# Kernel optimization log

Measured on AMD Instinct MI355X. Metric: run time of the kernel, lower is better.

Reference implementation:

```python
import jax, jax.numpy as jnp
import numpy as np

B, S, D = 16, 4096, 64
SCALE = float(np.sqrt(D))  # sqrt(hidden_size)


def setup_inputs() -> dict:
    key = jax.random.key(0)
    kq, kk, kv = jax.random.split(key, 3)
    return {
        "query": jax.random.normal(kq, (B, S, D), dtype=jnp.float32),
        "key": jax.random.normal(kk, (B, S, D), dtype=jnp.float32),
        "value": jax.random.normal(kv, (B, S, D), dtype=jnp.float32),
    }


def reference(query, key, value):
    # energy: [B, S, S]
    energy = jnp.einsum("bqd,bkd->bqk", query, key) / SCALE
    attention = jax.nn.softmax(energy, axis=2)
    return jnp.einsum("bqk,bkd->bqd", attention, value)
```

## Files before the change

kernel.cpp:

```cpp
#include <hip/hip_runtime.h>


#define NBATCH 16
#define SEQ    4096
#define DIM    64
#define BQ     256
#define BK     64
#define NKT    (SEQ / BK)
#define KHALF  (NKT / 2)
#define OELEMS (NBATCH * SEQ * DIM)
#define NROWS  (NBATCH * SEQ)
#define NTILES (NBATCH * NKT)
#define TILEH  4096

#define QSCALE 0.180336879f

typedef _Float16 half2_t __attribute__((ext_vector_type(2)));
typedef _Float16 half4_t __attribute__((ext_vector_type(4)));
typedef _Float16 half8_t __attribute__((ext_vector_type(8)));
typedef float    floatx4 __attribute__((ext_vector_type(4)));

__device__ inline float fast_exp2(float x) {
#if __has_builtin(__builtin_amdgcn_exp2f)
  return __builtin_amdgcn_exp2f(x);
#else
  return exp2f(x);
#endif
}
__device__ inline float fast_rcp(float x) {
#if __has_builtin(__builtin_amdgcn_rcpf)
  return __builtin_amdgcn_rcpf(x);
#else
  return 1.0f / x;
#endif
}

__device__ inline int swz(int row, int col) {
  return row * 64 + ((((col >> 3) ^ ((row >> 1) & 7)) << 3) | (col & 7));
}

__device__ inline void async16(const void* g, void* l) {
  __builtin_amdgcn_global_load_lds(
      (const __attribute__((address_space(1))) void*)g,
      (__attribute__((address_space(3))) void*)l, 16, 0, 0);
}

__global__ __launch_bounds__(256, 2)
void prepack_kv(const float* __restrict__ Kg, const float* __restrict__ Vg,
                _Float16* __restrict__ Kh, _Float16* __restrict__ Vh)
{
  __shared__ __align__(16) _Float16 sKi[TILEH];
  __shared__ __align__(16) _Float16 sVi[TILEH];
  const int tid = threadIdx.x;
  const int t16 = tid & 15;
  const int kg  = tid >> 4;
  const int bt  = blockIdx.x;
  const float* Kt_ = Kg + (size_t)bt * BK * DIM;
  const float* Vt_ = Vg + (size_t)bt * BK * DIM;

  floatx4 kbuf[4], vbuf[4];
  #pragma unroll
  for (int i = 0; i < 4; ++i) {
    const int key = kg + 16 * i;
    kbuf[i] = *(const floatx4*)(Kt_ + key * DIM + t16 * 4);
    vbuf[i] = *(const floatx4*)(Vt_ + key * DIM + t16 * 4);
  }
  #pragma unroll
  for (int i = 0; i < 4; ++i) {
    const int key = kg + 16 * i;
    half4_t h;
    #pragma unroll
    for (int j = 0; j < 4; ++j) h[j] = (_Float16)kbuf[i][j];
    *(half4_t*)&sKi[swz(key, t16 * 4)] = h;
  }
  {
    const int vbase = (kg >> 2) * 8 + (kg & 3) * 2;
    #pragma unroll
    for (int e = 0; e < 4; ++e) {
      const int dim = t16 * 4 + e;
      half2_t h0; h0[0] = (_Float16)vbuf[0][e]; h0[1] = (_Float16)vbuf[1][e];
      half2_t h1; h1[0] = (_Float16)vbuf[2][e]; h1[1] = (_Float16)vbuf[3][e];
      *(half2_t*)&sVi[swz(dim, vbase)]      = h0;
      *(half2_t*)&sVi[swz(dim, vbase + 32)] = h1;
    }
  }
  __syncthreads();
  half8_t* Ko = (half8_t*)(Kh + (size_t)bt * TILEH);
  half8_t* Vo = (half8_t*)(Vh + (size_t)bt * TILEH);
  const half8_t* Ks = (const half8_t*)sKi;
  const half8_t* Vs = (const half8_t*)sVi;
  Ko[tid] = Ks[tid]; Ko[tid + 256] = Ks[tid + 256];
  Vo[tid] = Vs[tid]; Vo[tid + 256] = Vs[tid + 256];
}

__global__ __launch_bounds__(256, 2)
void attn_f16_flash(const float* __restrict__ Qg, const _Float16* __restrict__ Kh,
                    const _Float16* __restrict__ Vh, float* __restrict__ O0g,
                    float* __restrict__ O1g, float* __restrict__ lsg)
{
  __shared__ __align__(16) _Float16 sT[4][2 * TILEH];

  const int tid  = threadIdx.x;
  const int wave = tid >> 6;
  const int lane = tid & 63;
  const int l16  = lane & 15;
  const int quad = lane >> 4;
  const int hK   = (l16 >> 1) & 7;

  const int bid  = blockIdx.x;
  const int x    = bid & 7;
  const int r    = bid >> 3;
  const int b    = x + ((r & 1) << 3);
  const int qt   = (r >> 1) & 15;
  const int half = (r >> 5) & 1;
  const int q0   = qt * BQ + wave * 64;
  const int kt0  = half * KHALF;

  const float* Qb = Qg + ((size_t)b * SEQ + q0) * DIM;
  float*       Ob = (half ? O1g : O0g) + ((size_t)b * SEQ + q0) * DIM;
  float*       Ls = lsg + (size_t)half * NROWS + b * SEQ + q0;

  half8_t qf[4][2];
  #pragma unroll
  for (int s = 0; s < 4; ++s)
    #pragma unroll
    for (int c = 0; c < 2; ++c) {
      const floatx4 f0 = *(const floatx4*)(Qb + (s * 16 + l16) * DIM + c * 32 + quad * 8);
      const floatx4 f1 = *(const floatx4*)(Qb + (s * 16 + l16) * DIM + c * 32 + quad * 8 + 4);
      half8_t h;
      #pragma unroll
      for (int j = 0; j < 4; ++j) h[j] = (_Float16)(f0[j] * QSCALE);
      #pragma unroll
      for (int j = 0; j < 4; ++j) h[4 + j] = (_Float16)(f1[j] * QSCALE);
      qf[s][c] = h;
    }

  floatx4 oacc2[4][4];
  float   lsum2[4];
  #pragma unroll
  for (int n = 0; n < 4; ++n)
    #pragma unroll
    for (int s = 0; s < 4; ++s) oacc2[n][s] = (floatx4){0.f, 0.f, 0.f, 0.f};
  #pragma unroll
  for (int s = 0; s < 4; ++s) lsum2[s] = 0.f;

  #define ASYNC(KT, BUF)                                                       \
    do {                                                                       \
      const char* gk = (const char*)(Kh + ((size_t)b * NKT + (KT)) * TILEH)    \
                       + wave * 2048;                                          \
      const char* gv = (const char*)(Vh + ((size_t)b * NKT + (KT)) * TILEH)    \
                       + wave * 2048;                                          \
      char* lk = (char*)(&sT[BUF][0])     + wave * 2048;                       \
      char* lv = (char*)(&sT[BUF][TILEH]) + wave * 2048;                       \
      async16(gk + lane * 16,        lk);                                      \
      async16(gk + 1024 + lane * 16, lk + 1024);                               \
      async16(gv + lane * 16,        lv);                                      \
      async16(gv + 1024 + lane * 16, lv + 1024);                               \
    } while (0)

  #define QKH(scX, BUF, H)                                                     \
    do {                                                                       \
      const _Float16* SKB = &sT[BUF][0];                                       \
      _Pragma("unroll")                                                        \
      for (int k2 = 0; k2 < 2; ++k2)                                           \
        _Pragma("unroll")                                                      \
        for (int s = 0; s < 4; ++s) scX[k2][s] = (floatx4){0.f, 0.f, 0.f, 0.f};\
      _Pragma("unroll")                                                        \
      for (int k2 = 0; k2 < 2; ++k2) {                                         \
        const int nk = (H) * 2 + k2;                                           \
        _Pragma("unroll")                                                      \
        for (int c = 0; c < 2; ++c) {                                          \
          half8_t kf = *(const half8_t*)&SKB[(nk * 16 + l16) * 64 +            \
                                             (((c * 4 + quad) ^ hK) << 3)];    \
          _Pragma("unroll")                                                    \
          for (int s = 0; s < 4; ++s)                                          \
            scX[k2][s] = __builtin_amdgcn_mfma_f32_16x16x32_f16(               \
                kf, qf[s][c], scX[k2][s], 0, 0, 0);                            \
        }                                                                      \
      }                                                                        \
    } while (0)

  #define EXPH(scX, bfrX)                                                      \
    do {                                                                       \
      _Pragma("unroll")                                                        \
      for (int s = 0; s < 4; ++s) {                                            \
        half8_t bf;                                                            \
        _Pragma("unroll")                                                      \
        for (int j = 0; j < 8; ++j) {                                          \
          float p = fast_exp2(scX[j & 1][s][j >> 1]);                          \
          lsum2[s] += p;                                                       \
          bf[j] = (_Float16)p;                                                 \
        }                                                                      \
        bfrX[s] = bf;                                                          \
      }                                                                        \
    } while (0)

  #define PVH(bfrX, BUF, H)                                                    \
    do {                                                                       \
      const _Float16* SVB = &sT[BUF][TILEH];                                   \
      _Pragma("unroll")                                                        \
      for (int n = 0; n < 4; ++n) {                                            \
        half8_t vf = *(const half8_t*)&SVB[(n * 16 + l16) * 64 +               \
                                           ((((H) * 4 + quad) ^ hK) << 3)];    \
        _Pragma("unroll")                                                      \
        for (int s = 0; s < 4; ++s)                                            \
          oacc2[n][s] = __builtin_amdgcn_mfma_f32_16x16x32_f16(                \
              vf, bfrX[s], oacc2[n][s], 0, 0, 0);                              \
      }                                                                        \
    } while (0)

  #define GATE(N)                                                              \
    do {                                                                       \
      asm volatile("s_waitcnt vmcnt(" #N ")" ::: "memory");                    \
      __builtin_amdgcn_s_barrier();                                            \
      __builtin_amdgcn_sched_barrier(0);                                       \
    } while (0)

  floatx4 scA[2][4], scB[2][4];
  half8_t bfrA[4], bfrB[4];

  ASYNC(kt0 + 0, 0);
  ASYNC(kt0 + 1, 1);
  GATE(4);
  ASYNC(kt0 + 2, 2);
  QKH(scA, 0, 0);

  #pragma unroll 1
  for (int t = 0; t < KHALF - 2; ++t) {
    const int cb = t & 3;
    QKH(scB, cb, 1);
    EXPH(scA, bfrA);
    PVH(bfrA, cb, 0);
    GATE(4);
    if (t + 3 < KHALF) ASYNC(kt0 + t + 3, (t + 3) & 3);
    QKH(scA, (t + 1) & 3, 0);
    EXPH(scB, bfrB);
    PVH(bfrB, cb, 1);
  }

  {
    const int cb = (KHALF - 2) & 3;
    QKH(scB, cb, 1);
    EXPH(scA, bfrA);
    PVH(bfrA, cb, 0);
    GATE(0);
    QKH(scA, (KHALF - 1) & 3, 0);
    EXPH(scB, bfrB);
    PVH(bfrB, cb, 1);
  }
  {
    const int cb = (KHALF - 1) & 3;
    QKH(scB, cb, 1);
    EXPH(scA, bfrA);
    PVH(bfrA, cb, 0);
    EXPH(scB, bfrB);
    PVH(bfrB, cb, 1);
  }

  #pragma unroll
  for (int s = 0; s < 4; ++s) {
    float v = lsum2[s];
    v += __shfl_xor(v, 16);
    v += __shfl_xor(v, 32);
    if (lane < 16) Ls[s * 16 + l16] = v;
  }
  #pragma unroll
  for (int s = 0; s < 4; ++s)
    #pragma unroll
    for (int n = 0; n < 4; ++n)
      *(floatx4*)&Ob[(s * 16 + l16) * DIM + n * 16 + quad * 4] = oacc2[n][s];

  #undef ASYNC
  #undef QKH
  #undef EXPH
  #undef PVH
  #undef GATE
}

__global__ __launch_bounds__(256)
void attn_combine(float* __restrict__ O, const float* __restrict__ O1,
                  const float* __restrict__ lsg)
{
  const int i = blockIdx.x * 256 + threadIdx.x;
  const int row = i >> 4;
  const float inv = fast_rcp(lsg[row] + lsg[NROWS + row]);
  const float4 a  = ((const float4*)O)[i];
  const float4 bb = ((const float4*)O1)[i];
  float4 r;
  r.x = (a.x + bb.x) * inv;
  r.y = (a.y + bb.y) * inv;
  r.z = (a.z + bb.z) * inv;
  r.w = (a.w + bb.w) * inv;
  ((float4*)O)[i] = r;
}

extern "C" void kernel_launch(void* const* d_in, const int* in_sizes, int n_in,
                              void* d_out, int out_size, void* d_ws, size_t ws_size,
                              hipStream_t stream) {
  const float* Q = (const float*)d_in[0];
  const float* K = (const float*)d_in[1];
  const float* V = (const float*)d_in[2];
  float* O  = (float*)d_out;
  (void)in_sizes; (void)n_in; (void)out_size; (void)ws_size;

  float*     O1 = (float*)d_ws;
  float*     Ls = O1 + OELEMS;
  _Float16*  Kh = (_Float16*)(Ls + 2 * NROWS);
  _Float16*  Vh = Kh + (size_t)NTILES * TILEH;

  prepack_kv<<<dim3(NTILES), dim3(256), 0, stream>>>(K, V, Kh, Vh);
  attn_f16_flash<<<dim3(2 * NBATCH * (SEQ / BQ)), dim3(256), 0, stream>>>(
      Q, Kh, Vh, O, O1, Ls);
  attn_combine<<<dim3(OELEMS / 4 / 256), dim3(256), 0, stream>>>(O, O1, Ls);
}
```

Measured before the change: 164.9 us.

## Fuse split-K combine into flash kernel via last-arriver atomic flag

Removes the separate combine kernel. Each of the two KV-half blocks for a query tile increments an atomic counter after writing its partial output and row sums, and the second block to arrive merges both partials and normalizes in place. This saves one kernel launch and a full extra pass over the output, at the cost of a memset, fences, an atomic per block, and a serial tail in whichever block finishes last.

```diff
diff --git a/kernel.cpp b/kernel.cpp
--- a/kernel.cpp
+++ b/kernel.cpp
@@ -12,6 +12,7 @@
 #define NROWS  (NBATCH * SEQ)
 #define NTILES (NBATCH * NKT)
 #define TILEH  4096
+#define NPAIR  (NBATCH * (SEQ / BQ))
 
 #define QSCALE 0.180336879f
 
@@ -96,7 +97,8 @@
 __global__ __launch_bounds__(256, 2)
 void attn_f16_flash(const float* __restrict__ Qg, const _Float16* __restrict__ Kh,
                     const _Float16* __restrict__ Vh, float* __restrict__ O0g,
-                    float* __restrict__ O1g, float* __restrict__ lsg)
+                    float* __restrict__ O1g, float* __restrict__ lsg,
+                    unsigned int* __restrict__ flags)
 {
   __shared__ __align__(16) _Float16 sT[4][2 * TILEH];
 
@@ -270,28 +272,40 @@
     for (int n = 0; n < 4; ++n)
       *(floatx4*)&Ob[(s * 16 + l16) * DIM + n * 16 + quad * 4] = oacc2[n][s];
 
+  __threadfence();
+  __syncthreads();
+  __shared__ unsigned int s_old;
+  if (tid == 0)
+    s_old = __hip_atomic_fetch_add(&flags[b * (SEQ / BQ) + qt], 1u,
+                                   __ATOMIC_ACQ_REL, __HIP_MEMORY_SCOPE_AGENT);
+  __syncthreads();
+  if (s_old == 1u) {
+    __threadfence();
+    const size_t rbase = (size_t)b * SEQ + qt * BQ;
+    float*       Of  = O0g + rbase * DIM;
+    const float* O1f = O1g + rbase * DIM;
+    const float* l0  = lsg + rbase;
+    const float* l1  = lsg + NROWS + rbase;
+    #pragma unroll 1
+    for (int i4 = tid; i4 < (BQ * DIM) / 4; i4 += 256) {
+      const int row = i4 >> 4;
+      const float inv = fast_rcp(l0[row] + l1[row]);
+      const float4 a  = ((const float4*)Of)[i4];
+      const float4 bb = ((const float4*)O1f)[i4];
+      float4 rr;
+      rr.x = (a.x + bb.x) * inv;
+      rr.y = (a.y + bb.y) * inv;
+      rr.z = (a.z + bb.z) * inv;
+      rr.w = (a.w + bb.w) * inv;
+      ((float4*)Of)[i4] = rr;
+    }
+  }
+
   #undef ASYNC
   #undef QKH
   #undef EXPH
   #undef PVH
   #undef GATE
-}
-
-__global__ __launch_bounds__(256)
-void attn_combine(float* __restrict__ O, const float* __restrict__ O1,
-                  const float* __restrict__ lsg)
-{
-  const int i = blockIdx.x * 256 + threadIdx.x;
-  const int row = i >> 4;
-  const float inv = fast_rcp(lsg[row] + lsg[NROWS + row]);
-  const float4 a  = ((const float4*)O)[i];
-  const float4 bb = ((const float4*)O1)[i];
-  float4 r;
-  r.x = (a.x + bb.x) * inv;
-  r.y = (a.y + bb.y) * inv;
-  r.z = (a.z + bb.z) * inv;
-  r.w = (a.w + bb.w) * inv;
-  ((float4*)O)[i] = r;
 }
 
 extern "C" void kernel_launch(void* const* d_in, const int* in_sizes, int n_in,
@@ -303,13 +317,14 @@
   float* O  = (float*)d_out;
   (void)in_sizes; (void)n_in; (void)out_size; (void)ws_size;
 
-  float*     O1 = (float*)d_ws;
-  float*     Ls = O1 + OELEMS;
-  _Float16*  Kh = (_Float16*)(Ls + 2 * NROWS);
-  _Float16*  Vh = Kh + (size_t)NTILES * TILEH;
-
+  float*        O1    = (float*)d_ws;
+  float*        Ls    = O1 + OELEMS;
+  unsigned int* flags = (unsigned int*)(Ls + 2 * NROWS);
+  _Float16*     Kh    = (_Float16*)(flags + NPAIR);
+  _Float16*     Vh    = Kh + (size_t)NTILES * TILEH;
+
+  hipMemsetAsync(flags, 0, NPAIR * sizeof(unsigned int), stream);
   prepack_kv<<<dim3(NTILES), dim3(256), 0, stream>>>(K, V, Kh, Vh);
   attn_f16_flash<<<dim3(2 * NBATCH * (SEQ / BQ)), dim3(256), 0, stream>>>(
-      Q, Kh, Vh, O, O1, Ls);
-  attn_combine<<<dim3(OELEMS / 4 / 256), dim3(256), 0, stream>>>(O, O1, Ls);
-}
+      Q, Kh, Vh, O, O1, Ls, flags);
+}
```

New measurement: 258.5 us. 56.8% more time.
